# Performance work log

Measured on AMD Instinct MI355X. Metric: run time of the kernel, lower is better.

The kernel has to match this reference:

```python
import jax, jax.numpy as jnp
import numpy as np

E1, E2, E3, M, DEC_H, OUT = 512, 512, 512, 1024, 2048, 1000
B = 16384

def _linear_params(key, fan_in, fan_out):
    kw, kb = jax.random.split(key)
    bound = 1.0 / np.sqrt(fan_in)
    W = jax.random.uniform(kw, (fan_out, fan_in), jnp.float32, -bound, bound)
    b = jax.random.uniform(kb, (fan_out,), jnp.float32, -bound, bound)
    return W, b

def setup_inputs() -> dict:
    key = jax.random.key(0)
    ks = jax.random.split(key, 7)
    tube = jax.random.normal(ks[0], (B, E1 + E2 + E3), jnp.float32)
    w1_W, w1_b = _linear_params(ks[1], E1, M)
    w2_W, w2_b = _linear_params(ks[2], E2, M)
    w3_W, w3_b = _linear_params(ks[3], E3, M)
    wh_W, wh_b = _linear_params(ks[4], 3 * M, M)
    wd1_W, wd1_b = _linear_params(ks[5], 2 * M, DEC_H)
    wd2_W, wd2_b = _linear_params(ks[6], DEC_H, OUT)
    return dict(tube=tube, w1_W=w1_W, w1_b=w1_b, w2_W=w2_W, w2_b=w2_b,
                w3_W=w3_W, w3_b=w3_b, wh_W=wh_W, wh_b=wh_b,
                wd1_W=wd1_W, wd1_b=wd1_b, wd2_W=wd2_W, wd2_b=wd2_b)

def reference(tube, w1_W, w1_b, w2_W, w2_b, w3_W, w3_b, wh_W, wh_b,
              wd1_W, wd1_b, wd2_W, wd2_b):
    relu = jax.nn.relu
    x1 = tube[:, :E1]
    x2 = tube[:, E1:E1 + E2]
    x3 = tube[:, E1 + E2:E1 + E2 + E3]
    P1 = relu(x1 @ w1_W.T + w1_b)   # [B, M]
    P2 = relu(x2 @ w2_W.T + w2_b)
    P3 = relu(x3 @ w3_W.T + w3_b)
    hid1 = jnp.concatenate([P1, P2, P3], axis=1)      # [B, 3M]
    last_hid = relu(hid1 @ wh_W.T + wh_b)             # [B, M]
    # diag(matmul(last_hid, P.T)) == row-wise dot product
    alpha1 = jnp.sum(last_hid * P1, axis=1)
    alpha2 = jnp.sum(last_hid * P2, axis=1)
    alpha3 = jnp.sum(last_hid * P3, axis=1)
    alphas = jnp.stack([alpha1, alpha2, alpha3], axis=1)  # [B, 3]
    weights = jax.nn.softmax(alphas, axis=1)
    context = (weights[:, 0:1] * P1 + weights[:, 1:2] * P2
               + weights[:, 2:3] * P3)                   # [B, M]
    decode_start = jnp.concatenate([context, last_hid], axis=1)  # [B, 2M]
    out = relu(decode_start @ wd1_W.T + wd1_b)
    out = out @ wd2_W.T + wd2_b                           # [B, OUT]
    return out
```

## Files before the change

### kernel.cpp

```cpp
#include <hip/hip_runtime.h>
#include <hip/hip_bf16.h>


typedef __bf16 bf16_t;
typedef __bf16 bf16x4 __attribute__((ext_vector_type(4)));
typedef __bf16 bf16x8 __attribute__((ext_vector_type(8)));
typedef float  f32x4  __attribute__((ext_vector_type(4)));

#define AS1(p) (const __attribute__((address_space(1))) void*)(p)
#define AS3(p) (__attribute__((address_space(3))) void*)(p)

__global__ void cvt_f32_bf16_v4(const float* __restrict__ src, bf16_t* __restrict__ dst,
                                int n4src, int n4tot) {
  for (int i = blockIdx.x * blockDim.x + threadIdx.x; i < n4tot; i += gridDim.x * blockDim.x) {
    bf16x4 o;
    if (i < n4src) {
      float4 f = ((const float4*)src)[i];
      o[0] = (bf16_t)f.x; o[1] = (bf16_t)f.y; o[2] = (bf16_t)f.z; o[3] = (bf16_t)f.w;
    } else {
      o[0] = (bf16_t)0.0f; o[1] = (bf16_t)0.0f; o[2] = (bf16_t)0.0f; o[3] = (bf16_t)0.0f;
    }
    *(bf16x4*)(dst + (size_t)i * 4) = o;
  }
}

__global__ void concat_bias3(const float* __restrict__ a, const float* __restrict__ b,
                             const float* __restrict__ c, float* __restrict__ dst) {
  int i = blockIdx.x * blockDim.x + threadIdx.x;
  if (i < 1024) dst[i] = a[i];
  else if (i < 2048) dst[i] = b[i - 1024];
  else if (i < 3072) dst[i] = c[i - 2048];
}

template<bool BDIAG, bool RELU, bool OUT_BF16>
__global__ __launch_bounds__(512, 2)
void gemm256(const bf16_t* __restrict__ A, int lda,
             const bf16_t* __restrict__ Bw, int ldb,
             const float* __restrict__ bias,
             void* __restrict__ Cout, int ldc,
             int K, int Nmask, int nbx)
{
  extern __shared__ char lds[];
  bf16_t* Ab = (bf16_t*)lds;
  bf16_t* Bb = (bf16_t*)(lds + 65536);

  const int t   = threadIdx.x;
  const int ln  = t & 63;
  const int w   = t >> 6;
  const int l15 = ln & 15, lhi = ln >> 4;
  const int wm  = w >> 2, wn = w & 3;

  const int nb = (int)gridDim.x;
  const int id = (int)blockIdx.x;
  const int id_sw = (id & 7) * (nb >> 3) + (id >> 3);
  const int bx = id_sw % nbx, by = id_sw / nbx;
  const int rowBase = by * 256;
  const int colBase = bx * 256;
  const int aCol0 = BDIAG ? (colBase >> 10) * 512 : 0;

  const int srow = (w << 4) + (ln >> 2);
  const int scol = (((ln & 3) ^ (ln >> 3)) & 3) << 3;

  const bf16_t* aS = A  + (size_t)(rowBase + srow) * lda + aCol0 + scol;
  const bf16_t* bS = Bw + (size_t)(colBase + srow) * ldb + scol;
  const size_t aI = (size_t)128 * lda;
  const size_t bI = (size_t)128 * ldb;
  bf16_t* daW = Ab + (w << 9);
  bf16_t* dbW = Bb + (w << 9);

  const int key  = (l15 >> 1) & 3;
  const int fcol = (lhi ^ key) << 3;
  const int aOff = (wm * 128 + l15) * 32 + fcol;
  const int bOff = (wn * 64  + l15) * 32 + fcol;

  const int nt = K >> 5;

  f32x4 acc[8][4] = {};

  #define STAGE(kt, s)                                                              \
    do {                                                                            \
      const bf16_t* a_ = aS + (size_t)(kt) * 32;                                    \
      const bf16_t* b_ = bS + (size_t)(kt) * 32;                                    \
      bf16_t* da_ = daW + (s) * 8192;                                               \
      bf16_t* db_ = dbW + (s) * 8192;                                               \
      __builtin_amdgcn_global_load_lds(AS1(a_),      AS3(da_),        16, 0, 0);    \
      __builtin_amdgcn_global_load_lds(AS1(a_ + aI), AS3(da_ + 4096), 16, 0, 0);    \
      __builtin_amdgcn_global_load_lds(AS1(b_),      AS3(db_),        16, 0, 0);    \
      __builtin_amdgcn_global_load_lds(AS1(b_ + bI), AS3(db_ + 4096), 16, 0, 0);    \
    } while (0)

  STAGE(0, 0); STAGE(1, 1); STAGE(2, 2);
  asm volatile("s_waitcnt vmcnt(8)" ::: "memory");
  __builtin_amdgcn_s_barrier();
  asm volatile("" ::: "memory");

  for (int j = 0; j < nt; ++j) {
    const int s = j & 3;
    bf16x8 af[8], bf[4];
    #pragma unroll
    for (int mf = 0; mf < 8; ++mf)
      af[mf] = *(const bf16x8*)(Ab + s * 8192 + aOff + mf * 512);
    #pragma unroll
    for (int nf = 0; nf < 4; ++nf)
      bf[nf] = *(const bf16x8*)(Bb + s * 8192 + bOff + nf * 512);

    if (j + 3 < nt) {
      STAGE(j + 3, ((j + 3) & 3));
      asm volatile("s_waitcnt vmcnt(8)" ::: "memory");
    } else if (j + 2 < nt) {
      asm volatile("s_waitcnt vmcnt(4)" ::: "memory");
    } else if (j + 1 < nt) {
      asm volatile("s_waitcnt vmcnt(0)" ::: "memory");
    }
    asm volatile("s_waitcnt lgkmcnt(0)" ::: "memory");
    __builtin_amdgcn_s_barrier();
    asm volatile("" ::: "memory");

    __builtin_amdgcn_s_setprio(1);
    #pragma unroll
    for (int mf = 0; mf < 8; ++mf)
      #pragma unroll
      for (int nf = 0; nf < 4; ++nf)
        acc[mf][nf] = __builtin_amdgcn_mfma_f32_16x16x32_bf16(af[mf], bf[nf], acc[mf][nf], 0, 0, 0);
    __builtin_amdgcn_s_setprio(0);
  }
  #undef STAGE

  #pragma unroll
  for (int mf = 0; mf < 8; ++mf) {
    const int row = rowBase + wm * 128 + mf * 16 + lhi * 4;
    #pragma unroll
    for (int nf = 0; nf < 4; ++nf) {
      const int col = colBase + wn * 64 + nf * 16 + l15;
      const float bv = (col < Nmask) ? bias[col] : 0.0f;
      #pragma unroll
      for (int i = 0; i < 4; ++i) {
        float v = acc[mf][nf][i] + bv;
        if (RELU) v = fmaxf(v, 0.0f);
        if (OUT_BF16) {
          ((bf16_t*)Cout)[(size_t)(row + i) * ldc + col] = (bf16_t)v;
        } else {
          if (col < Nmask) ((float*)Cout)[(size_t)(row + i) * ldc + col] = v;
        }
      }
    }
  }
}

__global__ __launch_bounds__(256)
void attn_ctx(const bf16_t* __restrict__ P, bf16_t* __restrict__ ds) {
  __shared__ float red[3][4];
  __shared__ float wsh[3];
  const int r = blockIdx.x;
  const int t = threadIdx.x;
  const bf16_t* Prow = P + (size_t)r * 3072;
  bf16_t* dsrow = ds + (size_t)r * 2048;

  const int j = t * 4;
  bf16x4 lv = *(const bf16x4*)(dsrow + 1024 + j);
  float lhv[4], pv[3][4];
  float s[3] = {0.f, 0.f, 0.f};
  #pragma unroll
  for (int q = 0; q < 4; q++) lhv[q] = (float)lv[q];
  #pragma unroll
  for (int e = 0; e < 3; e++) {
    bf16x4 p = *(const bf16x4*)(Prow + e * 1024 + j);
    #pragma unroll
    for (int q = 0; q < 4; q++) {
      pv[e][q] = (float)p[q];
      s[e] += lhv[q] * pv[e][q];
    }
  }
  #pragma unroll
  for (int off = 32; off > 0; off >>= 1) {
    #pragma unroll
    for (int e = 0; e < 3; e++) s[e] += __shfl_down(s[e], off, 64);
  }
  const int w = t >> 6, l = t & 63;
  if (l == 0) {
    #pragma unroll
    for (int e = 0; e < 3; e++) red[e][w] = s[e];
  }
  __syncthreads();
  if (t == 0) {
    float a0 = red[0][0] + red[0][1] + red[0][2] + red[0][3];
    float a1 = red[1][0] + red[1][1] + red[1][2] + red[1][3];
    float a2 = red[2][0] + red[2][1] + red[2][2] + red[2][3];
    float mx = fmaxf(a0, fmaxf(a1, a2));
    float e0 = expf(a0 - mx), e1 = expf(a1 - mx), e2 = expf(a2 - mx);
    float inv = 1.0f / (e0 + e1 + e2);
    wsh[0] = e0 * inv; wsh[1] = e1 * inv; wsh[2] = e2 * inv;
  }
  __syncthreads();
  const float w0 = wsh[0], w1 = wsh[1], w2 = wsh[2];
  bf16x4 o;
  #pragma unroll
  for (int q = 0; q < 4; q++)
    o[q] = (bf16_t)(w0 * pv[0][q] + w1 * pv[1][q] + w2 * pv[2][q]);
  *(bf16x4*)(dsrow + j) = o;
}

extern "C" void kernel_launch(void* const* d_in, const int* in_sizes, int n_in,
                              void* d_out, int out_size, void* d_ws, size_t ws_size,
                              hipStream_t stream) {
  (void)in_sizes; (void)n_in; (void)out_size; (void)ws_size;

  const float* tube = (const float*)d_in[0];
  const float* w1W  = (const float*)d_in[1];
  const float* w1b  = (const float*)d_in[2];
  const float* w2W  = (const float*)d_in[3];
  const float* w2b  = (const float*)d_in[4];
  const float* w3W  = (const float*)d_in[5];
  const float* w3b  = (const float*)d_in[6];
  const float* whW  = (const float*)d_in[7];
  const float* whb  = (const float*)d_in[8];
  const float* wd1W = (const float*)d_in[9];
  const float* wd1b = (const float*)d_in[10];
  const float* wd2W = (const float*)d_in[11];
  const float* wd2b = (const float*)d_in[12];

  char* ws = (char*)d_ws;
  bf16_t* P       = (bf16_t*)(ws + 0);
  bf16_t* ds      = (bf16_t*)(ws + 100663296);
  bf16_t* wd1B    = (bf16_t*)(ws + 167772160);
  bf16_t* wd2B    = (bf16_t*)(ws + 176160768);
  bf16_t* whB     = (bf16_t*)(ws + 180355072);
  bf16_t* w123B   = (bf16_t*)(ws + 186646528);
  bf16_t* tubeB   = (bf16_t*)(ws + 189792256);
  bf16_t* out1    = (bf16_t*)(ws + 180355072);
  float*  bias123 = (float*)(ws + 247463936);

  hipFuncSetAttribute((const void*)(gemm256<true,  true,  true >),
                      hipFuncAttributeMaxDynamicSharedMemorySize, 131072);
  hipFuncSetAttribute((const void*)(gemm256<false, true,  true >),
                      hipFuncAttributeMaxDynamicSharedMemorySize, 131072);
  hipFuncSetAttribute((const void*)(gemm256<false, false, false>),
                      hipFuncAttributeMaxDynamicSharedMemorySize, 131072);

  auto cvt = [&](const float* s, bf16_t* d, int n4s, int n4t) {
    int nb = (n4t + 255) / 256; if (nb > 2048) nb = 2048;
    hipLaunchKernelGGL(cvt_f32_bf16_v4, dim3(nb), dim3(256), 0, stream, s, d, n4s, n4t);
  };
  cvt(tube, tubeB, 6291456, 6291456);
  cvt(w1W,  w123B,           131072, 131072);
  cvt(w2W,  w123B +  524288, 131072, 131072);
  cvt(w3W,  w123B + 1048576, 131072, 131072);
  cvt(whW,  whB,  786432, 786432);
  cvt(wd1W, wd1B, 1048576, 1048576);
  cvt(wd2W, wd2B, 512000, 524288);
  hipLaunchKernelGGL(concat_bias3, dim3(12), dim3(256), 0, stream, w1b, w2b, w3b, bias123);

  hipLaunchKernelGGL((gemm256<true, true, true>), dim3(12 * 64), dim3(512), 131072, stream,
                     tubeB, 1536, w123B, 512, bias123, (void*)P, 3072, 512, 3072, 12);
  hipLaunchKernelGGL((gemm256<false, true, true>), dim3(4 * 64), dim3(512), 131072, stream,
                     P, 3072, whB, 3072, whb, (void*)(ds + 1024), 2048, 3072, 1024, 4);
  hipLaunchKernelGGL(attn_ctx, dim3(16384), dim3(256), 0, stream, P, ds);
  hipLaunchKernelGGL((gemm256<false, true, true>), dim3(8 * 64), dim3(512), 131072, stream,
                     ds, 2048, wd1B, 2048, wd1b, (void*)out1, 2048, 2048, 2048, 8);
  hipLaunchKernelGGL((gemm256<false, false, false>), dim3(4 * 64), dim3(512), 131072, stream,
                     out1, 2048, wd2B, 2048, wd2b, d_out, 1000, 2048, 1000, 4);
}
```

Measured before the change: 426.3 us.

## Double-buffer LDS fragment registers to overlap ds_reads with MFMA in GEMM loop

Restructures the GEMM main loop into a two-step unrolled ping-pong that keeps two sets of register fragments. The next k-slice's fragments are read from LDS while the current slice's MFMAs run. The wait counts and barrier placement are adjusted to match. The aim is to hide LDS read latency behind matrix-core work. The cost is higher register pressure, and the new loop assumes nt is even and that the 4-slot LDS ring stays race-free under the new waits.

```diff
diff --git a/kernel.cpp b/kernel.cpp
--- a/kernel.cpp
+++ b/kernel.cpp
@@ -76,6 +76,7 @@
   const int nt = K >> 5;
 
   f32x4 acc[8][4] = {};
+  bf16x8 afA[8], bfA[4], afB[8], bfB[4];
 
   #define STAGE(kt, s)                                                              \
     do {                                                                            \
@@ -89,42 +90,64 @@
       __builtin_amdgcn_global_load_lds(AS1(b_ + bI), AS3(db_ + 4096), 16, 0, 0);    \
     } while (0)
 
+  #define LOADFRAGS(slot, AF, BF)                                                   \
+    do {                                                                            \
+      const bf16_t* As_ = Ab + (slot) * 8192 + aOff;                                \
+      const bf16_t* Bs_ = Bb + (slot) * 8192 + bOff;                                \
+      _Pragma("unroll")                                                             \
+      for (int mf_ = 0; mf_ < 8; ++mf_) AF[mf_] = *(const bf16x8*)(As_ + mf_ * 512);\
+      _Pragma("unroll")                                                             \
+      for (int nf_ = 0; nf_ < 4; ++nf_) BF[nf_] = *(const bf16x8*)(Bs_ + nf_ * 512);\
+    } while (0)
+
+  #define MFMAC(AF, BF)                                                             \
+    do {                                                                            \
+      __builtin_amdgcn_s_setprio(1);                                                \
+      _Pragma("unroll")                                                             \
+      for (int mf_ = 0; mf_ < 8; ++mf_)                                             \
+        _Pragma("unroll")                                                           \
+        for (int nf_ = 0; nf_ < 4; ++nf_)                                           \
+          acc[mf_][nf_] = __builtin_amdgcn_mfma_f32_16x16x32_bf16(                  \
+              AF[mf_], BF[nf_], acc[mf_][nf_], 0, 0, 0);                            \
+      __builtin_amdgcn_s_setprio(0);                                                \
+    } while (0)
+
+  #define WAITS(x)                                                                  \
+    do {                                                                            \
+      if ((x) + 3 < nt) {                                                           \
+        asm volatile("s_waitcnt vmcnt(4)" ::: "memory");                            \
+        asm volatile("s_waitcnt lgkmcnt(0)" ::: "memory");                          \
+        __builtin_amdgcn_s_barrier();                                               \
+        asm volatile("" ::: "memory");                                              \
+      } else if ((x) + 2 < nt) {                                                    \
+        asm volatile("s_waitcnt vmcnt(0)" ::: "memory");                            \
+        asm volatile("s_waitcnt lgkmcnt(0)" ::: "memory");                          \
+        __builtin_amdgcn_s_barrier();                                               \
+        asm volatile("" ::: "memory");                                              \
+      }                                                                             \
+    } while (0)
+
   STAGE(0, 0); STAGE(1, 1); STAGE(2, 2);
-  asm volatile("s_waitcnt vmcnt(8)" ::: "memory");
+  asm volatile("s_waitcnt vmcnt(4)" ::: "memory");
   __builtin_amdgcn_s_barrier();
   asm volatile("" ::: "memory");
-
-  for (int j = 0; j < nt; ++j) {
-    const int s = j & 3;
-    bf16x8 af[8], bf[4];
-    #pragma unroll
-    for (int mf = 0; mf < 8; ++mf)
-      af[mf] = *(const bf16x8*)(Ab + s * 8192 + aOff + mf * 512);
-    #pragma unroll
-    for (int nf = 0; nf < 4; ++nf)
-      bf[nf] = *(const bf16x8*)(Bb + s * 8192 + bOff + nf * 512);
-
-    if (j + 3 < nt) {
-      STAGE(j + 3, ((j + 3) & 3));
-      asm volatile("s_waitcnt vmcnt(8)" ::: "memory");
-    } else if (j + 2 < nt) {
-      asm volatile("s_waitcnt vmcnt(4)" ::: "memory");
-    } else if (j + 1 < nt) {
-      asm volatile("s_waitcnt vmcnt(0)" ::: "memory");
-    }
-    asm volatile("s_waitcnt lgkmcnt(0)" ::: "memory");
-    __builtin_amdgcn_s_barrier();
-    asm volatile("" ::: "memory");
-
-    __builtin_amdgcn_s_setprio(1);
-    #pragma unroll
-    for (int mf = 0; mf < 8; ++mf)
-      #pragma unroll
-      for (int nf = 0; nf < 4; ++nf)
-        acc[mf][nf] = __builtin_amdgcn_mfma_f32_16x16x32_bf16(af[mf], bf[nf], acc[mf][nf], 0, 0, 0);
-    __builtin_amdgcn_s_setprio(0);
+  LOADFRAGS(0, afA, bfA);
+
+  for (int j = 0; j < nt; j += 2) {
+    if (j + 3 < nt) STAGE(j + 3, ((j + 3) & 3));
+    LOADFRAGS(((j + 1) & 3), afB, bfB);
+    MFMAC(afA, bfA);
+    WAITS(j);
+
+    if (j + 4 < nt) STAGE(j + 4, ((j + 4) & 3));
+    if (j + 2 < nt) LOADFRAGS(((j + 2) & 3), afA, bfA);
+    MFMAC(afB, bfB);
+    WAITS(j + 1);
   }
   #undef STAGE
+  #undef LOADFRAGS
+  #undef MFMAC
+  #undef WAITS
 
   #pragma unroll
   for (int mf = 0; mf < 8; ++mf) {
```

Measured after the change: 435.0 us. 1.02x slower.

## Restructure GEMM main loop into 8-phase ping-pong schedule with 64-wide K tiles

Applied to the files above, without the earlier changes.

Rewrites the GEMM mainloop to use 64-element K tiles with two LDS stages, each split into halves. Each half is loaded in a separate phase, and a 3-bit XOR swizzle is applied. Global-to-LDS loads for upcoming tiles are interleaved with LDS reads and MFMA blocks across eight barrier-separated phases per iteration. The aim is finer-grained overlap of memory traffic with matrix math and fewer waits per K element. In exchange it adds many more barriers per iteration and assumes nt is even.

```diff
diff --git a/kernel.cpp b/kernel.cpp
--- a/kernel.cpp
+++ b/kernel.cpp
@@ -41,8 +41,6 @@
              int K, int Nmask, int nbx)
 {
   extern __shared__ char lds[];
-  bf16_t* Ab = (bf16_t*)lds;
-  bf16_t* Bb = (bf16_t*)(lds + 65536);
 
   const int t   = threadIdx.x;
   const int ln  = t & 63;
@@ -58,73 +56,122 @@
   const int colBase = bx * 256;
   const int aCol0 = BDIAG ? (colBase >> 10) * 512 : 0;
 
-  const int srow = (w << 4) + (ln >> 2);
-  const int scol = (((ln & 3) ^ (ln >> 3)) & 3) << 3;
-
-  const bf16_t* aS = A  + (size_t)(rowBase + srow) * lda + aCol0 + scol;
-  const bf16_t* bS = Bw + (size_t)(colBase + srow) * ldb + scol;
-  const size_t aI = (size_t)128 * lda;
-  const size_t bI = (size_t)128 * ldb;
-  bf16_t* daW = Ab + (w << 9);
-  bf16_t* dbW = Bb + (w << 9);
-
-  const int key  = (l15 >> 1) & 3;
-  const int fcol = (lhi ^ key) << 3;
-  const int aOff = (wm * 128 + l15) * 32 + fcol;
-  const int bOff = (wn * 64  + l15) * 32 + fcol;
-
-  const int nt = K >> 5;
+  const int swcol = (((ln & 7) ^ (ln >> 3)) & 7) << 3;
+  const bf16_t* srcA = A  + (size_t)(rowBase + 8 * w + (ln >> 3)) * lda + aCol0 + swcol;
+  const bf16_t* srcB = Bw + (size_t)(colBase + 8 * w + (ln >> 3)) * ldb + swcol;
+  char* ldsA_w = lds + w * 1024;
+  char* ldsB_w = lds + 65536 + w * 1024;
+
+  const int aRd0 = wm * 8192 + l15 * 128 + (((0 * 4 + lhi) ^ (l15 & 7)) << 4);
+  const int aRd1 = wm * 8192 + l15 * 128 + (((1 * 4 + lhi) ^ (l15 & 7)) << 4);
+  const int bRd0 = (wn >> 1) * 16384 + (wn & 1) * 8192 + l15 * 128 + (((0 * 4 + lhi) ^ (l15 & 7)) << 4);
+  const int bRd1 = (wn >> 1) * 16384 + (wn & 1) * 8192 + l15 * 128 + (((1 * 4 + lhi) ^ (l15 & 7)) << 4);
+
+  const int nt = K >> 6;
+  const int ni = nt >> 1;
 
   f32x4 acc[8][4] = {};
-
-  #define STAGE(kt, s)                                                              \
-    do {                                                                            \
-      const bf16_t* a_ = aS + (size_t)(kt) * 32;                                    \
-      const bf16_t* b_ = bS + (size_t)(kt) * 32;                                    \
-      bf16_t* da_ = daW + (s) * 8192;                                               \
-      bf16_t* db_ = dbW + (s) * 8192;                                               \
-      __builtin_amdgcn_global_load_lds(AS1(a_),      AS3(da_),        16, 0, 0);    \
-      __builtin_amdgcn_global_load_lds(AS1(a_ + aI), AS3(da_ + 4096), 16, 0, 0);    \
-      __builtin_amdgcn_global_load_lds(AS1(b_),      AS3(db_),        16, 0, 0);    \
-      __builtin_amdgcn_global_load_lds(AS1(b_ + bI), AS3(db_ + 4096), 16, 0, 0);    \
-    } while (0)
-
-  STAGE(0, 0); STAGE(1, 1); STAGE(2, 2);
-  asm volatile("s_waitcnt vmcnt(8)" ::: "memory");
+  bf16x8 aR[4], bR0[4], bR1[4];
+
+  #define STAGE_A(s, h, tile)                                                          \
+    do {                                                                               \
+      const bf16_t* p_ = srcA + (size_t)(64 * (h)) * lda + (size_t)(tile) * 64;        \
+      char* d_ = ldsA_w + (s) * 32768 + (h) * 16384;                                   \
+      __builtin_amdgcn_global_load_lds(AS1(p_), AS3(d_), 16, 0, 0);                    \
+      __builtin_amdgcn_global_load_lds(AS1(p_ + (size_t)128 * lda), AS3(d_ + 8192), 16, 0, 0); \
+    } while (0)
+
+  #define STAGE_B(s, h, tile)                                                          \
+    do {                                                                               \
+      const bf16_t* p_ = srcB + (size_t)(128 * (h)) * ldb + (size_t)(tile) * 64;       \
+      char* d_ = ldsB_w + (s) * 32768 + (h) * 16384;                                   \
+      __builtin_amdgcn_global_load_lds(AS1(p_), AS3(d_), 16, 0, 0);                    \
+      __builtin_amdgcn_global_load_lds(AS1(p_ + (size_t)64 * ldb), AS3(d_ + 8192), 16, 0, 0); \
+    } while (0)
+
+  #define LD_A(s, h, AOFF)                                                             \
+    do {                                                                               \
+      const char* p_ = lds + (s) * 32768 + (h) * 16384 + (AOFF);                       \
+      aR[0] = *(const bf16x8*)(p_);        aR[1] = *(const bf16x8*)(p_ + 2048);        \
+      aR[2] = *(const bf16x8*)(p_ + 4096); aR[3] = *(const bf16x8*)(p_ + 6144);        \
+    } while (0)
+
+  #define LD_B(s, BOFF, BR)                                                            \
+    do {                                                                               \
+      const char* p_ = lds + 65536 + (s) * 32768 + (BOFF);                             \
+      BR[0] = *(const bf16x8*)(p_);        BR[1] = *(const bf16x8*)(p_ + 2048);        \
+      BR[2] = *(const bf16x8*)(p_ + 4096); BR[3] = *(const bf16x8*)(p_ + 6144);        \
+    } while (0)
+
+  #define MM(H, BR)                                                                    \
+    do {                                                                               \
+      __builtin_amdgcn_s_setprio(1);                                                   \
+      _Pragma("unroll")                                                                \
+      for (int m_ = 0; m_ < 4; ++m_)                                                   \
+        _Pragma("unroll")                                                              \
+        for (int n_ = 0; n_ < 4; ++n_)                                                 \
+          acc[(H) * 4 + m_][n_] = __builtin_amdgcn_mfma_f32_16x16x32_bf16(             \
+              aR[m_], BR[n_], acc[(H) * 4 + m_][n_], 0, 0, 0);                         \
+      __builtin_amdgcn_s_setprio(0);                                                   \
+    } while (0)
+
+  #define BAR_MID()                                                                    \
+    do {                                                                               \
+      __builtin_amdgcn_s_barrier();                                                    \
+      asm volatile("s_waitcnt lgkmcnt(0)" ::: "memory");                               \
+      __builtin_amdgcn_sched_barrier(0);                                               \
+    } while (0)
+
+  #define BAR_END()                                                                    \
+    do { __builtin_amdgcn_s_barrier(); asm volatile("" ::: "memory"); } while (0)
+
+  STAGE_A(0, 0, 0); STAGE_B(0, 0, 0); STAGE_A(0, 1, 0); STAGE_B(0, 1, 0);
+  STAGE_A(1, 0, 1); STAGE_B(1, 0, 1);
+  asm volatile("s_waitcnt vmcnt(4)" ::: "memory");
   __builtin_amdgcn_s_barrier();
   asm volatile("" ::: "memory");
 
-  for (int j = 0; j < nt; ++j) {
-    const int s = j & 3;
-    bf16x8 af[8], bf[4];
-    #pragma unroll
-    for (int mf = 0; mf < 8; ++mf)
-      af[mf] = *(const bf16x8*)(Ab + s * 8192 + aOff + mf * 512);
-    #pragma unroll
-    for (int nf = 0; nf < 4; ++nf)
-      bf[nf] = *(const bf16x8*)(Bb + s * 8192 + bOff + nf * 512);
-
-    if (j + 3 < nt) {
-      STAGE(j + 3, ((j + 3) & 3));
-      asm volatile("s_waitcnt vmcnt(8)" ::: "memory");
-    } else if (j + 2 < nt) {
-      asm volatile("s_waitcnt vmcnt(4)" ::: "memory");
-    } else if (j + 1 < nt) {
-      asm volatile("s_waitcnt vmcnt(0)" ::: "memory");
-    }
-    asm volatile("s_waitcnt lgkmcnt(0)" ::: "memory");
-    __builtin_amdgcn_s_barrier();
-    asm volatile("" ::: "memory");
-
-    __builtin_amdgcn_s_setprio(1);
-    #pragma unroll
-    for (int mf = 0; mf < 8; ++mf)
-      #pragma unroll
-      for (int nf = 0; nf < 4; ++nf)
-        acc[mf][nf] = __builtin_amdgcn_mfma_f32_16x16x32_bf16(af[mf], bf[nf], acc[mf][nf], 0, 0, 0);
-    __builtin_amdgcn_s_setprio(0);
-  }
-  #undef STAGE
+  for (int i = 0; i < ni; ++i) {
+    const bool nl = (i + 1 < ni);
+    const int t1 = 2 * i + 1, t2 = 2 * i + 2, t3 = 2 * i + 3;
+
+    LD_A(0, 0, aRd0); LD_B(0, bRd0, bR0);
+    STAGE_A(1, 1, t1);
+    BAR_MID(); MM(0, bR0); BAR_END();
+    LD_A(0, 0, aRd1); LD_B(0, bRd1, bR1);
+    STAGE_B(1, 1, t1);
+    BAR_MID(); MM(0, bR1); BAR_END();
+    LD_A(0, 1, aRd0);
+    if (nl) STAGE_A(0, 0, t2);
+    BAR_MID(); MM(1, bR0); BAR_END();
+    LD_A(0, 1, aRd1);
+    if (nl) STAGE_B(0, 0, t2);
+    BAR_MID(); MM(1, bR1);
+    if (nl) { asm volatile("s_waitcnt vmcnt(4)" ::: "memory"); }
+    else    { asm volatile("s_waitcnt vmcnt(0)" ::: "memory"); }
+    BAR_END();
+    LD_A(1, 0, aRd0); LD_B(1, bRd0, bR0);
+    if (nl) STAGE_A(0, 1, t2);
+    BAR_MID(); MM(0, bR0); BAR_END();
+    LD_A(1, 0, aRd1); LD_B(1, bRd1, bR1);
+    if (nl) STAGE_B(0, 1, t2);
+    BAR_MID(); MM(0, bR1); BAR_END();
+    LD_A(1, 1, aRd0);
+    if (nl) STAGE_A(1, 0, t3);
+    BAR_MID(); MM(1, bR0); BAR_END();
+    LD_A(1, 1, aRd1);
+    if (nl) STAGE_B(1, 0, t3);
+    BAR_MID(); MM(1, bR1);
+    if (nl) { asm volatile("s_waitcnt vmcnt(4)" ::: "memory"); }
+    BAR_END();
+  }
+  #undef STAGE_A
+  #undef STAGE_B
+  #undef LD_A
+  #undef LD_B
+  #undef MM
+  #undef BAR_MID
+  #undef BAR_END
 
   #pragma unroll
   for (int mf = 0; mf < 8; ++mf) {
```

Result: no change. 420.6 us (-1.3%).

## Switch GEMMs to 128x128 tiles with double-buffered static LDS

Applied to the files above, without the earlier changes.

Replaces the 256x256-tile, 512-thread GEMM with a 128x128-tile, 256-thread kernel using static LDS and two-stage double buffering. Grids are enlarged accordingly, so more blocks are resident per CU. The aim is better occupancy and wave-level latency hiding. In exchange it gives up the deeper 4-stage prefetch pipeline and the MFMA priority hints, and halves data reuse per tile, which increases global/L2 traffic.

```diff
diff --git a/kernel.cpp b/kernel.cpp
--- a/kernel.cpp
+++ b/kernel.cpp
@@ -33,105 +33,89 @@
 }
 
 template<bool BDIAG, bool RELU, bool OUT_BF16>
-__global__ __launch_bounds__(512, 2)
-void gemm256(const bf16_t* __restrict__ A, int lda,
+__global__ __launch_bounds__(256, 4)
+void gemm128(const bf16_t* __restrict__ A, int lda,
              const bf16_t* __restrict__ Bw, int ldb,
              const float* __restrict__ bias,
              void* __restrict__ Cout, int ldc,
              int K, int Nmask, int nbx)
 {
-  extern __shared__ char lds[];
-  bf16_t* Ab = (bf16_t*)lds;
-  bf16_t* Bb = (bf16_t*)(lds + 65536);
+  __shared__ __attribute__((aligned(16))) bf16_t As[2][4096];
+  __shared__ __attribute__((aligned(16))) bf16_t Bs[2][4096];
 
   const int t   = threadIdx.x;
   const int ln  = t & 63;
+  const int l15 = ln & 15, lhi = ln >> 4;
   const int w   = t >> 6;
-  const int l15 = ln & 15, lhi = ln >> 4;
-  const int wm  = w >> 2, wn = w & 3;
+  const int wr  = w >> 1, wc = w & 1;
 
   const int nb = (int)gridDim.x;
   const int id = (int)blockIdx.x;
   const int id_sw = (id & 7) * (nb >> 3) + (id >> 3);
   const int bx = id_sw % nbx, by = id_sw / nbx;
-  const int rowBase = by * 256;
-  const int colBase = bx * 256;
+  const int rowBase = by * 128;
+  const int colBase = bx * 128;
   const int aCol0 = BDIAG ? (colBase >> 10) * 512 : 0;
 
-  const int srow = (w << 4) + (ln >> 2);
-  const int scol = (((ln & 3) ^ (ln >> 3)) & 3) << 3;
-
-  const bf16_t* aS = A  + (size_t)(rowBase + srow) * lda + aCol0 + scol;
-  const bf16_t* bS = Bw + (size_t)(colBase + srow) * ldb + scol;
-  const size_t aI = (size_t)128 * lda;
-  const size_t bI = (size_t)128 * ldb;
-  bf16_t* daW = Ab + (w << 9);
-  bf16_t* dbW = Bb + (w << 9);
+  const int r0   = t >> 2;
+  const int scol = (((t & 3) ^ ((t >> 3) & 3)) & 3) << 3;
+  const bf16_t* aS = A  + (size_t)(rowBase + r0) * lda + aCol0 + scol;
+  const bf16_t* bS = Bw + (size_t)(colBase + r0) * ldb + scol;
+  const size_t aI = (size_t)64 * lda;
+  const size_t bI = (size_t)64 * ldb;
 
   const int key  = (l15 >> 1) & 3;
   const int fcol = (lhi ^ key) << 3;
-  const int aOff = (wm * 128 + l15) * 32 + fcol;
-  const int bOff = (wn * 64  + l15) * 32 + fcol;
+  const int aOff = (wr * 64 + l15) * 32 + fcol;
+  const int bOff = (wc * 64 + l15) * 32 + fcol;
 
   const int nt = K >> 5;
 
-  f32x4 acc[8][4] = {};
+  f32x4 acc[4][4] = {};
 
   #define STAGE(kt, s)                                                              \
     do {                                                                            \
       const bf16_t* a_ = aS + (size_t)(kt) * 32;                                    \
       const bf16_t* b_ = bS + (size_t)(kt) * 32;                                    \
-      bf16_t* da_ = daW + (s) * 8192;                                               \
-      bf16_t* db_ = dbW + (s) * 8192;                                               \
+      char* da_ = (char*)As[s] + t * 16;                                            \
+      char* db_ = (char*)Bs[s] + t * 16;                                            \
       __builtin_amdgcn_global_load_lds(AS1(a_),      AS3(da_),        16, 0, 0);    \
       __builtin_amdgcn_global_load_lds(AS1(a_ + aI), AS3(da_ + 4096), 16, 0, 0);    \
       __builtin_amdgcn_global_load_lds(AS1(b_),      AS3(db_),        16, 0, 0);    \
       __builtin_amdgcn_global_load_lds(AS1(b_ + bI), AS3(db_ + 4096), 16, 0, 0);    \
     } while (0)
 
-  STAGE(0, 0); STAGE(1, 1); STAGE(2, 2);
-  asm volatile("s_waitcnt vmcnt(8)" ::: "memory");
-  __builtin_amdgcn_s_barrier();
-  asm volatile("" ::: "memory");
+  STAGE(0, 0);
+  __syncthreads();
 
   for (int j = 0; j < nt; ++j) {
-    const int s = j & 3;
-    bf16x8 af[8], bf[4];
-    #pragma unroll
-    for (int mf = 0; mf < 8; ++mf)
-      af[mf] = *(const bf16x8*)(Ab + s * 8192 + aOff + mf * 512);
-    #pragma unroll
-    for (int nf = 0; nf < 4; ++nf)
-      bf[nf] = *(const bf16x8*)(Bb + s * 8192 + bOff + nf * 512);
-
-    if (j + 3 < nt) {
-      STAGE(j + 3, ((j + 3) & 3));
-      asm volatile("s_waitcnt vmcnt(8)" ::: "memory");
-    } else if (j + 2 < nt) {
-      asm volatile("s_waitcnt vmcnt(4)" ::: "memory");
-    } else if (j + 1 < nt) {
-      asm volatile("s_waitcnt vmcnt(0)" ::: "memory");
-    }
-    asm volatile("s_waitcnt lgkmcnt(0)" ::: "memory");
-    __builtin_amdgcn_s_barrier();
-    asm volatile("" ::: "memory");
-
-    __builtin_amdgcn_s_setprio(1);
-    #pragma unroll
-    for (int mf = 0; mf < 8; ++mf)
+    const int s = j & 1;
+    if (j + 1 < nt) STAGE(j + 1, s ^ 1);
+
+    const bf16_t* As_ = As[s] + aOff;
+    const bf16_t* Bs_ = Bs[s] + bOff;
+    bf16x8 af[4], bfr[4];
+    #pragma unroll
+    for (int mf = 0; mf < 4; ++mf) af[mf] = *(const bf16x8*)(As_ + mf * 512);
+    #pragma unroll
+    for (int nf = 0; nf < 4; ++nf) bfr[nf] = *(const bf16x8*)(Bs_ + nf * 512);
+
+    #pragma unroll
+    for (int mf = 0; mf < 4; ++mf)
       #pragma unroll
       for (int nf = 0; nf < 4; ++nf)
-        acc[mf][nf] = __builtin_amdgcn_mfma_f32_16x16x32_bf16(af[mf], bf[nf], acc[mf][nf], 0, 0, 0);
-    __builtin_amdgcn_s_setprio(0);
+        acc[mf][nf] = __builtin_amdgcn_mfma_f32_16x16x32_bf16(af[mf], bfr[nf], acc[mf][nf], 0, 0, 0);
+
+    __syncthreads();
   }
   #undef STAGE
 
   #pragma unroll
-  for (int mf = 0; mf < 8; ++mf) {
-    const int row = rowBase + wm * 128 + mf * 16 + lhi * 4;
+  for (int mf = 0; mf < 4; ++mf) {
+    const int row = rowBase + wr * 64 + mf * 16 + lhi * 4;
     #pragma unroll
     for (int nf = 0; nf < 4; ++nf) {
-      const int col = colBase + wn * 64 + nf * 16 + l15;
+      const int col = colBase + wc * 64 + nf * 16 + l15;
       const float bv = (col < Nmask) ? bias[col] : 0.0f;
       #pragma unroll
       for (int i = 0; i < 4; ++i) {
@@ -230,13 +214,6 @@
   bf16_t* out1    = (bf16_t*)(ws + 180355072);
   float*  bias123 = (float*)(ws + 247463936);
 
-  hipFuncSetAttribute((const void*)(gemm256<true,  true,  true >),
-                      hipFuncAttributeMaxDynamicSharedMemorySize, 131072);
-  hipFuncSetAttribute((const void*)(gemm256<false, true,  true >),
-                      hipFuncAttributeMaxDynamicSharedMemorySize, 131072);
-  hipFuncSetAttribute((const void*)(gemm256<false, false, false>),
-                      hipFuncAttributeMaxDynamicSharedMemorySize, 131072);
-
   auto cvt = [&](const float* s, bf16_t* d, int n4s, int n4t) {
     int nb = (n4t + 255) / 256; if (nb > 2048) nb = 2048;
     hipLaunchKernelGGL(cvt_f32_bf16_v4, dim3(nb), dim3(256), 0, stream, s, d, n4s, n4t);
@@ -250,13 +227,13 @@
   cvt(wd2W, wd2B, 512000, 524288);
   hipLaunchKernelGGL(concat_bias3, dim3(12), dim3(256), 0, stream, w1b, w2b, w3b, bias123);
 
-  hipLaunchKernelGGL((gemm256<true, true, true>), dim3(12 * 64), dim3(512), 131072, stream,
-                     tubeB, 1536, w123B, 512, bias123, (void*)P, 3072, 512, 3072, 12);
-  hipLaunchKernelGGL((gemm256<false, true, true>), dim3(4 * 64), dim3(512), 131072, stream,
-                     P, 3072, whB, 3072, whb, (void*)(ds + 1024), 2048, 3072, 1024, 4);
+  hipLaunchKernelGGL((gemm128<true, true, true>), dim3(24 * 128), dim3(256), 0, stream,
+                     tubeB, 1536, w123B, 512, bias123, (void*)P, 3072, 512, 3072, 24);
+  hipLaunchKernelGGL((gemm128<false, true, true>), dim3(8 * 128), dim3(256), 0, stream,
+                     P, 3072, whB, 3072, whb, (void*)(ds + 1024), 2048, 3072, 1024, 8);
   hipLaunchKernelGGL(attn_ctx, dim3(16384), dim3(256), 0, stream, P, ds);
-  hipLaunchKernelGGL((gemm256<false, true, true>), dim3(8 * 64), dim3(512), 131072, stream,
-                     ds, 2048, wd1B, 2048, wd1b, (void*)out1, 2048, 2048, 2048, 8);
-  hipLaunchKernelGGL((gemm256<false, false, false>), dim3(4 * 64), dim3(512), 131072, stream,
-                     out1, 2048, wd2B, 2048, wd2b, d_out, 1000, 2048, 1000, 4);
-}
+  hipLaunchKernelGGL((gemm128<false, true, true>), dim3(16 * 128), dim3(256), 0, stream,
+                     ds, 2048, wd1B, 2048, wd1b, (void*)out1, 2048, 2048, 2048, 16);
+  hipLaunchKernelGGL((gemm128<false, false, false>), dim3(8 * 128), dim3(256), 0, stream,
+                     out1, 2048, wd2B, 2048, wd2b, d_out, 1000, 2048, 1000, 8);
+}
```

New measurement: 499.1 us. +17.1%, slower.
